# Performance work log

Hardware: AMD Instinct MI355X
Metric: run time of the kernel (lower is better)

The kernel has to match this reference:

```python
import jax, jax.numpy as jnp
import numpy as np
import math

B, S, D, H, HD = 2, 2048, 2048, 16, 128
ROPE_THETA = 10000.0


def _rope_cache(seq_len, dim, base, dtype=jnp.float32):
    inv_freq = 1.0 / (base ** (jnp.arange(0, dim, 2, dtype=jnp.float32) / dim))
    t = jnp.arange(seq_len, dtype=jnp.float32)
    freqs = jnp.einsum('i,j->ij', t, inv_freq)          # [S, dim/2]
    emb = jnp.concatenate([freqs, freqs], axis=-1)       # [S, dim]
    return jnp.cos(emb).astype(dtype), jnp.sin(emb).astype(dtype)


def _rotate_half(x):
    x1, x2 = x[..., : x.shape[-1] // 2], x[..., x.shape[-1] // 2:]
    return jnp.concatenate([-x2, x1], axis=-1)


def setup_inputs() -> dict:
    key = jax.random.key(0)
    ks = jax.random.split(key, 6)
    hidden_states = jax.random.normal(ks[0], (B, S, D), dtype=jnp.float32) * 0.02
    w_scale = 1.0 / math.sqrt(D)
    Wq = jax.random.normal(ks[1], (D, D), dtype=jnp.float32) * w_scale
    Wk = jax.random.normal(ks[2], (D, D), dtype=jnp.float32) * w_scale
    Wv = jax.random.normal(ks[3], (D, D), dtype=jnp.float32) * w_scale
    Wo = jax.random.normal(ks[4], (D, D), dtype=jnp.float32) * w_scale
    # additive causal mask [B, 1, S, S]: 0 on/below diag, large negative above
    causal = jnp.tril(jnp.ones((S, S), dtype=bool))
    attention_mask = jnp.where(causal, 0.0, -1e9).astype(jnp.float32)
    attention_mask = jnp.broadcast_to(attention_mask[None, None], (B, 1, S, S))
    position_ids = jnp.broadcast_to(jnp.arange(S, dtype=jnp.int32)[None], (B, S))
    return {
        'hidden_states': hidden_states,
        'attention_mask': attention_mask,
        'position_ids': position_ids,
        'Wq': Wq, 'Wk': Wk, 'Wv': Wv, 'Wo': Wo,
    }


def reference(hidden_states, attention_mask, position_ids, Wq, Wk, Wv, Wo):
    bsz, q_len, _ = hidden_states.shape
    # projections (torch Linear: x @ W.T), then split heads -> [B, H, S, HD]
    def proj(W):
        return jnp.einsum('bsd,ed->bse', hidden_states, W).reshape(bsz, q_len, H, HD).transpose(0, 2, 1, 3)
    q, k, v = proj(Wq), proj(Wk), proj(Wv)
    cos_c, sin_c = _rope_cache(q_len, HD, ROPE_THETA, hidden_states.dtype)
    cos = cos_c[position_ids][:, None]  # [B, 1, S, HD]
    sin = sin_c[position_ids][:, None]
    q = q * cos + _rotate_half(q) * sin
    k = k * cos + _rotate_half(k) * sin
    scores = jnp.einsum('bhqd,bhkd->bhqk', q, k) / math.sqrt(HD)
    scores = scores + attention_mask
    attn_weights = jax.nn.softmax(scores.astype(jnp.float32), axis=-1).astype(q.dtype)
    attn_out = jnp.einsum('bhqk,bhkd->bhqd', attn_weights, v)
    attn_out = attn_out.transpose(0, 2, 1, 3).reshape(bsz, q_len, D)
    out = jnp.einsum('bsd,ed->bse', attn_out, Wo)
    return out
```

## Files before the change

kernel.cpp:

```cpp
#include <hip/hip_runtime.h>

typedef __bf16 bf16;
typedef __bf16 bf16x8 __attribute__((ext_vector_type(8)));
typedef float f32x4 __attribute__((ext_vector_type(4)));

#define D_MODEL 2048
#define SEQ 2048
#define NH 16
#define HEAD_DIM 128
#define NBATCH 2
#define SM_SCALE 0.08838834764831845f
#define WSEG 4194304
#define NT_TILES 32

typedef __attribute__((address_space(1))) const void* gas_cp;
typedef __attribute__((address_space(3))) void* las_p;
__device__ __forceinline__ void ll16(const bf16* g, bf16* l) {
  __builtin_amdgcn_global_load_lds((gas_cp)g, (las_p)l, 16, 0, 0);
}

__device__ __forceinline__ bf16x8 cvt8(const float* p) {
  float4 a = *(const float4*)p;
  float4 b = *(const float4*)(p + 4);
  bf16x8 v;
  v[0] = (bf16)a.x; v[1] = (bf16)a.y; v[2] = (bf16)a.z; v[3] = (bf16)a.w;
  v[4] = (bf16)b.x; v[5] = (bf16)b.y; v[6] = (bf16)b.z; v[7] = (bf16)b.w;
  return v;
}

__global__ __launch_bounds__(256)
void cvt_hidden(const float* __restrict__ src, bf16* __restrict__ dst) {
  size_t i = ((size_t)blockIdx.x * 256 + threadIdx.x) * 8;
  *(bf16x8*)(dst + i) = cvt8(src + i);
}

__global__ __launch_bounds__(256)
void cvt_weights(const float* __restrict__ w0, const float* __restrict__ w1,
                 const float* __restrict__ w2, const float* __restrict__ w3,
                 bf16* __restrict__ dst) {
  const float* src = (blockIdx.y == 0) ? w0 : (blockIdx.y == 1) ? w1
                   : (blockIdx.y == 2) ? w2 : w3;
  size_t i = ((size_t)blockIdx.x * 256 + threadIdx.x) * 8;
  *(bf16x8*)(dst + (size_t)blockIdx.y * WSEG + i) = cvt8(src + i);
}

#define LDF256(DA, DB, SB, KX)                                               \
  _Pragma("unroll") for (int mi = 0; mi < 8; mi++)                           \
      DA[mi] = *(const bf16x8*)((SB) + ((arowQ + mi * 16) << 7) + (KX));     \
  DB[0] = *(const bf16x8*)((SB) + 32768 + (qb0 << 7) + (KX));                \
  DB[1] = *(const bf16x8*)((SB) + 32768 + (qb1 << 7) + (KX));                \
  DB[2] = *(const bf16x8*)((SB) + 32768 + (qb2 << 7) + (KX));                \
  DB[3] = *(const bf16x8*)((SB) + 32768 + (qb3 << 7) + (KX));

#define MM256(AF, BF)                                                        \
  _Pragma("unroll") for (int mi = 0; mi < 8; mi++)                           \
  _Pragma("unroll") for (int ni = 0; ni < 4; ni++)                           \
      acc[mi][ni] = __builtin_amdgcn_mfma_f32_16x16x32_bf16(                 \
          AF[mi], BF[ni], acc[mi][ni], 0, 0, 0);

#define ST2(GP, ROW0, KT, LB)                                                \
  ll16((GP) + (size_t)((ROW0) + w * 8 + l8) * D_MODEL + (KT) * 64 + kelem,   \
       (bf16*)((LB) + w * 1024));

__global__ __launch_bounds__(512, 2)
void gemm256(const bf16* __restrict__ A, const bf16* __restrict__ W,
             bf16* __restrict__ Qo, bf16* __restrict__ Ko,
             bf16* __restrict__ Vo, const int* __restrict__ pos_ids) {
  __shared__ __align__(16) char smem[131072];

  const int tid  = threadIdx.x;
  const int lane = tid & 63;
  const int w    = tid >> 6;
  const int quad = lane >> 4, l15 = lane & 15;
  const int l8   = lane >> 3, l7 = lane & 7;
  const int kelem = 8 * (l7 ^ l8);
  const int wm2 = w >> 2;
  const int wn2 = w & 3;
  const int hh  = wn2 >> 1;
  const int cb  = (wn2 & 1) * 32;

  const int bid = blockIdx.x;
  const int lin = (bid & 7) * 48 + (bid >> 3);
  const int by = lin / 24, bx = lin % 24;
  const int mBase = by << 8, nBase = bx << 8;

  const int kx0 = (quad * 16) ^ ((l15 & 7) << 4);
  const int kx1 = kx0 ^ 64;
  const int arowQ = wm2 * 128 + l15;
  const int qb0 = hh * 128 + cb + l15;
  const int qb1 = qb0 + 16, qb2 = qb0 + 64, qb3 = qb0 + 80;

  f32x4 acc[8][4];
#pragma unroll
  for (int i = 0; i < 8; i++)
#pragma unroll
    for (int j = 0; j < 4; j++) acc[i][j] = 0.0f;

  bf16x8 aP[8], bP[4];
  bf16x8 aQ[8], bQ[4];

  {
    char* s0 = smem;
    ST2(A, mBase,       0, s0 + 0);
    ST2(A, mBase + 64,  0, s0 + 8192);
    ST2(A, mBase + 128, 0, s0 + 16384);
    ST2(A, mBase + 192, 0, s0 + 24576);
    ST2(W, nBase,       0, s0 + 32768);
    ST2(W, nBase + 64,  0, s0 + 40960);
    ST2(W, nBase + 128, 0, s0 + 49152);
    ST2(W, nBase + 192, 0, s0 + 57344);
  }
  asm volatile("s_waitcnt vmcnt(0)" ::: "memory");
  __builtin_amdgcn_s_barrier();
  LDF256(aP, bP, smem, kx0);

  int buf = 0;
  for (int t = 0; t < NT_TILES; ++t) {
    char* const Sb = smem + buf * 65536;
    char* const Ob = smem + (buf ^ 1) * 65536;
    const bool pf  = (t + 1 < NT_TILES);

    LDF256(aQ, bQ, Sb, kx1);
    if (pf) {
      ST2(A, mBase,       t + 1, Ob + 0);
      ST2(A, mBase + 64,  t + 1, Ob + 8192);
      ST2(A, mBase + 128, t + 1, Ob + 16384);
      ST2(A, mBase + 192, t + 1, Ob + 24576);
      ST2(W, nBase,       t + 1, Ob + 32768);
      ST2(W, nBase + 64,  t + 1, Ob + 40960);
      ST2(W, nBase + 128, t + 1, Ob + 49152);
      ST2(W, nBase + 192, t + 1, Ob + 57344);
    }
    __builtin_amdgcn_sched_barrier(0);
    __builtin_amdgcn_s_setprio(1);
    MM256(aP, bP);
    __builtin_amdgcn_s_setprio(0);
    asm volatile("s_waitcnt lgkmcnt(0)" ::: "memory");
    asm volatile("s_waitcnt vmcnt(0)" ::: "memory");
    __builtin_amdgcn_s_barrier();

    if (pf) {
      LDF256(aP, bP, Ob, kx0);
    }
    __builtin_amdgcn_sched_barrier(0);
    __builtin_amdgcn_s_setprio(1);
    MM256(aQ, bQ);
    __builtin_amdgcn_s_setprio(0);
    asm volatile("s_waitcnt lgkmcnt(0)" ::: "memory");

    buf ^= 1;
  }

  const int matrix = nBase >> 11;
  const int nb     = nBase & 2047;
  if (matrix == 2) {
    const int h = (nb >> 7) + hh;
#pragma unroll
    for (int mi = 0; mi < 8; mi++)
#pragma unroll
      for (int ni = 0; ni < 4; ni++) {
        const int hd = cb + (ni & 1) * 16 + (ni >> 1) * 64 + l15;
#pragma unroll
        for (int r = 0; r < 4; r++) {
          int m = mBase + wm2 * 128 + mi * 16 + quad * 4 + r;
          int b = m >> 11, s2 = m & 2047;
          Vo[((size_t)((b * NH + h) * HEAD_DIM + hd)) * SEQ + s2] =
              (bf16)acc[mi][ni][r];
        }
      }
  } else {
    bf16* Out = (matrix == 0) ? Qo : Ko;
    float invf[2];
#pragma unroll
    for (int ni = 0; ni < 2; ni++)
      invf[ni] = __expf(-(float)(cb + ni * 16 + l15) *
                        (9.210340371976184f / 64.0f));
#pragma unroll
    for (int mi = 0; mi < 8; mi++)
#pragma unroll
      for (int r = 0; r < 4; r++) {
        int m = mBase + wm2 * 128 + mi * 16 + quad * 4 + r;
        float pos = (float)pos_ids[m];
        bf16* op = Out + (size_t)m * D_MODEL + nb + hh * 128 + cb + l15;
#pragma unroll
        for (int ni = 0; ni < 2; ni++) {
          float sn, cs;
          __sincosf(pos * invf[ni], &sn, &cs);
          float q0 = acc[mi][ni][r];
          float q1 = acc[mi][ni + 2][r];
          op[ni * 16]      = (bf16)(q0 * cs - q1 * sn);
          op[ni * 16 + 64] = (bf16)(q1 * cs + q0 * sn);
        }
      }
  }
}

#define LDFRAG(DA, DB, SB, KX)                                               \
  _Pragma("unroll") for (int mi = 0; mi < 4; mi++)                           \
      DA[mi] = *(const bf16x8*)((SB) + ((arow + mi * 16) << 7) + (KX));      \
  DB[0] = *(const bf16x8*)((SB) + 16384 + (rb0 << 7) + (KX));                \
  DB[1] = *(const bf16x8*)((SB) + 16384 + (rb1 << 7) + (KX));                \
  DB[2] = *(const bf16x8*)((SB) + 16384 + (rb2 << 7) + (KX));                \
  DB[3] = *(const bf16x8*)((SB) + 16384 + (rb3 << 7) + (KX));

#define MMAC(AF, BF)                                                         \
  _Pragma("unroll") for (int mi = 0; mi < 4; mi++)                           \
  _Pragma("unroll") for (int ni = 0; ni < 4; ni++)                           \
      acc[mi][ni] = __builtin_amdgcn_mfma_f32_16x16x32_bf16(                 \
          AF[mi], BF[ni], acc[mi][ni], 0, 0, 0);

#define ST1(GP, ROW0, KT, LB)                                                \
  ll16((GP) + (size_t)((ROW0) + w * 8 + l8) * D_MODEL + (KT) * 64 + kelem,   \
       (bf16*)((LB) + w * 1024));

__global__ __launch_bounds__(512, 2)
void gemm_proj(const bf16* __restrict__ A, const bf16* __restrict__ W,
               float* __restrict__ C) {
  __shared__ __align__(16) char smem[147456];

  const int tid  = threadIdx.x;
  const int lane = tid & 63;
  const int w    = tid >> 6;
  const int quad = lane >> 4, l15 = lane & 15;
  const int l8   = lane >> 3, l7 = lane & 7;
  const int kelem = 8 * (l7 ^ l8);
  const int wm = w >> 2;
  const int wn = w & 3;

  const int bid = blockIdx.x;
  const int lin = (bid & 7) * 32 + (bid >> 3);
  const int by = lin >> 3, bx = lin & 7;
  const int mBase = by << 7, nBase = bx << 8;

  const int kx0 = (quad * 16) ^ ((l15 & 7) << 4);
  const int kx1 = kx0 ^ 64;
  const int arow = wm * 64 + l15;
  const int rb0 = wn * 64 + l15;
  const int rb1 = rb0 + 16, rb2 = rb0 + 32, rb3 = rb0 + 48;

  f32x4 acc[4][4];
#pragma unroll
  for (int i = 0; i < 4; i++)
#pragma unroll
    for (int j = 0; j < 4; j++) acc[i][j] = 0.0f;

  bf16x8 aP[4], bP[4], aQ[4], bQ[4];

  {
    char* s0 = smem;
    char* s1 = smem + 49152;
    ST1(A, mBase,       0, s0 + 0);
    ST1(A, mBase + 64,  0, s0 + 8192);
    ST1(W, nBase,       0, s0 + 16384);
    ST1(W, nBase + 64,  0, s0 + 24576);
    ST1(W, nBase + 128, 0, s0 + 32768);
    ST1(W, nBase + 192, 0, s0 + 40960);
    ST1(A, mBase,       1, s1 + 0);
    ST1(A, mBase + 64,  1, s1 + 8192);
    ST1(W, nBase,       1, s1 + 16384);
    ST1(W, nBase + 64,  1, s1 + 24576);
    ST1(W, nBase + 128, 1, s1 + 32768);
    ST1(W, nBase + 192, 1, s1 + 40960);
  }
  asm volatile("s_waitcnt vmcnt(6)" ::: "memory");
  __builtin_amdgcn_s_barrier();
  LDFRAG(aP, bP, smem, kx0);

  int buf = 0;
  for (int t = 0; t < NT_TILES; ++t) {
    char* const Sb  = smem + buf * 49152;
    const int  nb1  = (buf + 1 == 3) ? 0 : buf + 1;
    const int  pb   = (buf + 2 >= 3) ? buf - 1 : buf + 2;
    char* const Nb  = smem + nb1 * 49152;
    char* const Pb  = smem + pb * 49152;
    const bool pf   = (t + 2 < NT_TILES);

    LDFRAG(aQ, bQ, Sb, kx1);
    if (pf) {
      ST1(A, mBase,      t + 2, Pb + 0);
      ST1(A, mBase + 64, t + 2, Pb + 8192);
      ST1(W, nBase,      t + 2, Pb + 16384);
    }
    __builtin_amdgcn_sched_barrier(0);
    __builtin_amdgcn_s_setprio(1);
    MMAC(aP, bP);
    __builtin_amdgcn_s_setprio(0);
    asm volatile("s_waitcnt lgkmcnt(0)" ::: "memory");
    if (pf)
      asm volatile("s_waitcnt vmcnt(3)" ::: "memory");
    else
      asm volatile("s_waitcnt vmcnt(0)" ::: "memory");
    __builtin_amdgcn_s_barrier();

    if (t + 1 < NT_TILES) {
      LDFRAG(aP, bP, Nb, kx0);
    }
    if (pf) {
      ST1(W, nBase + 64,  t + 2, Pb + 24576);
      ST1(W, nBase + 128, t + 2, Pb + 32768);
      ST1(W, nBase + 192, t + 2, Pb + 40960);
    }
    __builtin_amdgcn_sched_barrier(0);
    __builtin_amdgcn_s_setprio(1);
    MMAC(aQ, bQ);
    __builtin_amdgcn_s_setprio(0);
    asm volatile("s_waitcnt lgkmcnt(0)" ::: "memory");
    __builtin_amdgcn_s_barrier();

    buf = nb1;
  }

#pragma unroll
  for (int mi = 0; mi < 4; mi++) {
    const int m = mBase + wm * 64 + mi * 16 + quad * 4;
#pragma unroll
    for (int ni = 0; ni < 4; ni++) {
      const int n = nBase + wn * 64 + ni * 16 + l15;
      float* cp = C + (size_t)m * D_MODEL + n;
#pragma unroll
      for (int r = 0; r < 4; r++) cp[(size_t)r * D_MODEL] = acc[mi][ni][r];
    }
  }
}

__global__ __launch_bounds__(256, 1)
void attn_v3(const bf16* __restrict__ Q, const bf16* __restrict__ K,
             const bf16* __restrict__ Vt, bf16* __restrict__ O) {
  __shared__ __align__(16) bf16 Kl[2][64 * 128];
  __shared__ __align__(16) bf16 Vl[2][128 * 64];
  __shared__ __align__(16) bf16 Pl[128 * 64];

  const int tid  = threadIdx.x;
  const int lane = tid & 63;
  const int w    = tid >> 6;
  const int quad = lane >> 4, l15 = lane & 15;
  const int l8   = lane >> 3, l7 = lane & 7;
  const int jj   = blockIdx.y;
  const int bh   = blockIdx.x;
  const size_t qkBase = (size_t)(bh >> 4) * SEQ * D_MODEL + (size_t)(bh & 15) * HEAD_DIM;
  const size_t vBase  = (size_t)bh * HEAD_DIM * SEQ;
  const int kswz = (l15 & 7) << 3;
  const int prow = w * 32;

  bf16x8 ones;
#pragma unroll
  for (int i = 0; i < 8; i++) ones[i] = (bf16)1.0f;

#define STAGE_KV(T0, BUF)                                                    \
  _Pragma("unroll") for (int i_ = 0; i_ < 4; i_++) {                         \
    const int u_ = w * 4 + i_;                                               \
    const int rK = u_ * 4 + quad;                                            \
    ll16(K + qkBase + (size_t)((T0) + rK) * D_MODEL + 8 * (l15 ^ (rK & 7)),  \
         &Kl[BUF][u_ * 512]);                                                \
    const int rV = u_ * 8 + l8;                                              \
    ll16(Vt + vBase + (size_t)rV * SEQ + (T0) + 8 * (l7 ^ (rV & 7)),         \
         &Vl[BUF][u_ * 512]);                                                \
  }

#pragma unroll 1
  for (int ss = 0; ss < 2; ++ss) {
    const int s   = ss ? jj : 15 - jj;
    const int qbw = s * 128 + prow;
    const int nt  = 2 * s + 2;

    bf16x8 qa[2][4];
#pragma unroll
    for (int mi = 0; mi < 2; mi++)
#pragma unroll
      for (int kk = 0; kk < 4; kk++)
        qa[mi][kk] = *(const bf16x8*)(Q + qkBase +
            (size_t)(qbw + mi * 16 + l15) * D_MODEL + kk * 32 + quad * 8);

    f32x4 oacc[2][8], ls[2];
#pragma unroll
    for (int mi = 0; mi < 2; mi++) {
#pragma unroll
      for (int ni = 0; ni < 8; ni++) oacc[mi][ni] = 0.0f;
      ls[mi] = 0.0f;
    }

    STAGE_KV(0, 0);
    asm volatile("s_waitcnt vmcnt(0)" ::: "memory");
    __builtin_amdgcn_s_barrier();

    int cur = 0;
    for (int tt = 0; tt < nt; ++tt, cur ^= 1) {
      const int t0 = tt * 64;
      if (tt + 1 < nt) STAGE_KV(t0 + 64, cur ^ 1);

      if (t0 <= qbw + 31) {
        const bf16* Kc = &Kl[cur][0];
        const bf16* Vc = &Vl[cur][0];

        f32x4 sacc[2][4];
#pragma unroll
        for (int mi = 0; mi < 2; mi++)
#pragma unroll
          for (int ni = 0; ni < 4; ni++) sacc[mi][ni] = 0.0f;
#pragma unroll
        for (int kk = 0; kk < 4; kk++) {
#pragma unroll
          for (int ni = 0; ni < 4; ni++) {
            bf16x8 kf = *(const bf16x8*)&Kc[(ni * 16 + l15) * 128 +
                                            ((kk * 32 + quad * 8) ^ kswz)];
            sacc[0][ni] = __builtin_amdgcn_mfma_f32_16x16x32_bf16(qa[0][kk], kf, sacc[0][ni], 0, 0, 0);
            sacc[1][ni] = __builtin_amdgcn_mfma_f32_16x16x32_bf16(qa[1][kk], kf, sacc[1][ni], 0, 0, 0);
          }
        }

        if (t0 + 63 > qbw) {
#pragma unroll
          for (int mi = 0; mi < 2; mi++)
#pragma unroll
            for (int r = 0; r < 4; r++) {
              const int qrow = qbw + mi * 16 + quad * 4 + r;
              const int prr  = prow + mi * 16 + quad * 4 + r;
              const int rsw  = ((quad * 4 + r) & 7) << 3;
#pragma unroll
              for (int ni = 0; ni < 4; ni++) {
                int tcol = t0 + ni * 16 + l15;
                float pv = (tcol <= qrow)
                    ? __expf(fminf(sacc[mi][ni][r] * SM_SCALE, 30.0f)) : 0.0f;
                Pl[prr * 64 + ((ni * 16 + l15) ^ rsw)] = (bf16)pv;
              }
            }
        } else {
#pragma unroll
          for (int mi = 0; mi < 2; mi++)
#pragma unroll
            for (int r = 0; r < 4; r++) {
              const int prr = prow + mi * 16 + quad * 4 + r;
              const int rsw = ((quad * 4 + r) & 7) << 3;
#pragma unroll
              for (int ni = 0; ni < 4; ni++)
                Pl[prr * 64 + ((ni * 16 + l15) ^ rsw)] =
                    (bf16)__expf(fminf(sacc[mi][ni][r] * SM_SCALE, 30.0f));
            }
        }

#pragma unroll
        for (int kk2 = 0; kk2 < 2; kk2++) {
          const int pcol = (kk2 * 32 + quad * 8) ^ kswz;
          bf16x8 pf0 = *(const bf16x8*)&Pl[(prow + l15) * 64 + pcol];
          bf16x8 pf1 = *(const bf16x8*)&Pl[(prow + 16 + l15) * 64 + pcol];
#pragma unroll
          for (int ni = 0; ni < 8; ni++) {
            bf16x8 vf = *(const bf16x8*)&Vc[(ni * 16 + l15) * 64 + pcol];
            oacc[0][ni] = __builtin_amdgcn_mfma_f32_16x16x32_bf16(pf0, vf, oacc[0][ni], 0, 0, 0);
            oacc[1][ni] = __builtin_amdgcn_mfma_f32_16x16x32_bf16(pf1, vf, oacc[1][ni], 0, 0, 0);
          }
          ls[0] = __builtin_amdgcn_mfma_f32_16x16x32_bf16(pf0, ones, ls[0], 0, 0, 0);
          ls[1] = __builtin_amdgcn_mfma_f32_16x16x32_bf16(pf1, ones, ls[1], 0, 0, 0);
        }
      }

      asm volatile("s_waitcnt vmcnt(0)" ::: "memory");
      __builtin_amdgcn_s_barrier();
    }

#pragma unroll
    for (int mi = 0; mi < 2; mi++)
#pragma unroll
      for (int r = 0; r < 4; r++) {
        float inv = 1.0f / ls[mi][r];
        bf16* op = O + qkBase + (size_t)(qbw + mi * 16 + quad * 4 + r) * D_MODEL;
#pragma unroll
        for (int ni = 0; ni < 8; ni++)
          op[ni * 16 + l15] = (bf16)(oacc[mi][ni][r] * inv);
      }
  }
#undef STAGE_KV
}

extern "C" void kernel_launch(void* const* d_in, const int* in_sizes, int n_in,
                              void* d_out, int out_size, void* d_ws, size_t ws_size,
                              hipStream_t stream) {
  const float* hidden = (const float*)d_in[0];
  const int* pos = (const int*)d_in[2];
  const float* Wq = (const float*)d_in[3];
  const float* Wk = (const float*)d_in[4];
  const float* Wv = (const float*)d_in[5];
  const float* Wo = (const float*)d_in[6];
  float* out = (float*)d_out;

  const size_t TENS = (size_t)NBATCH * SEQ * D_MODEL;
  bf16* Qb = (bf16*)d_ws;
  bf16* Kb = Qb + TENS;
  bf16* Vt = Kb + TENS;
  bf16* AO = Vt + TENS;
  bf16* Hb = AO + TENS;
  bf16* Wb = Hb + TENS;

  cvt_hidden<<<dim3(TENS / 2048), dim3(256), 0, stream>>>(hidden, Hb);
  cvt_weights<<<dim3(WSEG / 2048, 4), dim3(256), 0, stream>>>(Wq, Wk, Wv, Wo, Wb);

  gemm256<<<dim3(384), dim3(512), 0, stream>>>(Hb, Wb, Qb, Kb, Vt, pos);

  attn_v3<<<dim3(NBATCH * NH, 8), dim3(256), 0, stream>>>(Qb, Kb, Vt, AO);

  gemm_proj<<<dim3(256), dim3(512), 0, stream>>>(
      AO, Wb + 3 * (size_t)WSEG, out);
}
```

Baseline: 377.9 us.

## Split each attention KV tile across two wave groups and reduce partial outputs

The attention kernel grows from 256 to 512 threads. The second group of four waves takes the other 32-key half of each 64-key tile, so each wave does half the QK^T and PV MFMAs per tile. The two halves' partial O accumulators and row sums are combined through shared memory at the end of each query block. The grid stays the same (256 blocks), so the aim is more waves per CU to hide latency. The cost is an extra shared-memory reduction with barriers and a larger shared-memory footprint.

```diff
diff --git a/kernel.cpp b/kernel.cpp
--- a/kernel.cpp
+++ b/kernel.cpp
@@ -323,38 +323,41 @@
   }
 }
 
-__global__ __launch_bounds__(256, 1)
-void attn_v3(const bf16* __restrict__ Q, const bf16* __restrict__ K,
+__global__ __launch_bounds__(512, 2)
+void attn_v4(const bf16* __restrict__ Q, const bf16* __restrict__ K,
              const bf16* __restrict__ Vt, bf16* __restrict__ O) {
-  __shared__ __align__(16) bf16 Kl[2][64 * 128];
-  __shared__ __align__(16) bf16 Vl[2][128 * 64];
-  __shared__ __align__(16) bf16 Pl[128 * 64];
+  __shared__ __align__(16) char smem[98304];
+  bf16* const KlB = (bf16*)smem;
+  bf16* const VlB = (bf16*)(smem + 32768);
+  bf16* const Pl  = (bf16*)(smem + 65536);
 
   const int tid  = threadIdx.x;
   const int lane = tid & 63;
   const int w    = tid >> 6;
   const int quad = lane >> 4, l15 = lane & 15;
   const int l8   = lane >> 3, l7 = lane & 7;
+  const int g    = w & 3;
+  const int h    = w >> 2;
   const int jj   = blockIdx.y;
   const int bh   = blockIdx.x;
   const size_t qkBase = (size_t)(bh >> 4) * SEQ * D_MODEL + (size_t)(bh & 15) * HEAD_DIM;
   const size_t vBase  = (size_t)bh * HEAD_DIM * SEQ;
   const int kswz = (l15 & 7) << 3;
-  const int prow = w * 32;
+  const int prow = g * 32;
 
   bf16x8 ones;
 #pragma unroll
   for (int i = 0; i < 8; i++) ones[i] = (bf16)1.0f;
 
 #define STAGE_KV(T0, BUF)                                                    \
-  _Pragma("unroll") for (int i_ = 0; i_ < 4; i_++) {                         \
-    const int u_ = w * 4 + i_;                                               \
+  _Pragma("unroll") for (int i_ = 0; i_ < 2; i_++) {                         \
+    const int u_ = w * 2 + i_;                                               \
     const int rK = u_ * 4 + quad;                                            \
     ll16(K + qkBase + (size_t)((T0) + rK) * D_MODEL + 8 * (l15 ^ (rK & 7)),  \
-         &Kl[BUF][u_ * 512]);                                                \
+         KlB + (BUF) * 8192 + u_ * 512);                                     \
     const int rV = u_ * 8 + l8;                                              \
     ll16(Vt + vBase + (size_t)rV * SEQ + (T0) + 8 * (l7 ^ (rV & 7)),         \
-         &Vl[BUF][u_ * 512]);                                                \
+         VlB + (BUF) * 8192 + u_ * 512);                                     \
   }
 
 #pragma unroll 1
@@ -389,19 +392,19 @@
       if (tt + 1 < nt) STAGE_KV(t0 + 64, cur ^ 1);
 
       if (t0 <= qbw + 31) {
-        const bf16* Kc = &Kl[cur][0];
-        const bf16* Vc = &Vl[cur][0];
-
-        f32x4 sacc[2][4];
+        const bf16* Kc = KlB + cur * 8192;
+        const bf16* Vc = VlB + cur * 8192;
+
+        f32x4 sacc[2][2];
 #pragma unroll
         for (int mi = 0; mi < 2; mi++)
 #pragma unroll
-          for (int ni = 0; ni < 4; ni++) sacc[mi][ni] = 0.0f;
+          for (int ni = 0; ni < 2; ni++) sacc[mi][ni] = 0.0f;
 #pragma unroll
         for (int kk = 0; kk < 4; kk++) {
 #pragma unroll
-          for (int ni = 0; ni < 4; ni++) {
-            bf16x8 kf = *(const bf16x8*)&Kc[(ni * 16 + l15) * 128 +
+          for (int ni = 0; ni < 2; ni++) {
+            bf16x8 kf = *(const bf16x8*)&Kc[(h * 32 + ni * 16 + l15) * 128 +
                                             ((kk * 32 + quad * 8) ^ kswz)];
             sacc[0][ni] = __builtin_amdgcn_mfma_f32_16x16x32_bf16(qa[0][kk], kf, sacc[0][ni], 0, 0, 0);
             sacc[1][ni] = __builtin_amdgcn_mfma_f32_16x16x32_bf16(qa[1][kk], kf, sacc[1][ni], 0, 0, 0);
@@ -417,11 +420,12 @@
               const int prr  = prow + mi * 16 + quad * 4 + r;
               const int rsw  = ((quad * 4 + r) & 7) << 3;
 #pragma unroll
-              for (int ni = 0; ni < 4; ni++) {
-                int tcol = t0 + ni * 16 + l15;
+              for (int ni = 0; ni < 2; ni++) {
+                const int col = h * 32 + ni * 16 + l15;
+                const int tcol = t0 + col;
                 float pv = (tcol <= qrow)
                     ? __expf(fminf(sacc[mi][ni][r] * SM_SCALE, 30.0f)) : 0.0f;
-                Pl[prr * 64 + ((ni * 16 + l15) ^ rsw)] = (bf16)pv;
+                Pl[prr * 64 + (col ^ rsw)] = (bf16)pv;
               }
             }
         } else {
@@ -432,15 +436,16 @@
               const int prr = prow + mi * 16 + quad * 4 + r;
               const int rsw = ((quad * 4 + r) & 7) << 3;
 #pragma unroll
-              for (int ni = 0; ni < 4; ni++)
-                Pl[prr * 64 + ((ni * 16 + l15) ^ rsw)] =
+              for (int ni = 0; ni < 2; ni++) {
+                const int col = h * 32 + ni * 16 + l15;
+                Pl[prr * 64 + (col ^ rsw)] =
                     (bf16)__expf(fminf(sacc[mi][ni][r] * SM_SCALE, 30.0f));
+              }
             }
         }
 
-#pragma unroll
-        for (int kk2 = 0; kk2 < 2; kk2++) {
-          const int pcol = (kk2 * 32 + quad * 8) ^ kswz;
+        {
+          const int pcol = (h * 32 + quad * 8) ^ kswz;
           bf16x8 pf0 = *(const bf16x8*)&Pl[(prow + l15) * 64 + pcol];
           bf16x8 pf1 = *(const bf16x8*)&Pl[(prow + 16 + l15) * 64 + pcol];
 #pragma unroll
@@ -458,16 +463,47 @@
       __builtin_amdgcn_s_barrier();
     }
 
-#pragma unroll
-    for (int mi = 0; mi < 2; mi++)
-#pragma unroll
-      for (int r = 0; r < 4; r++) {
-        float inv = 1.0f / ls[mi][r];
-        bf16* op = O + qkBase + (size_t)(qbw + mi * 16 + quad * 4 + r) * D_MODEL;
-#pragma unroll
-        for (int ni = 0; ni < 8; ni++)
-          op[ni * 16 + l15] = (bf16)(oacc[mi][ni][r] * inv);
+    float* const Ml = (float*)smem;
+    float* const Ls = (float*)(smem + 81920);
+    if (h == 1) {
+#pragma unroll
+      for (int mi = 0; mi < 2; mi++)
+#pragma unroll
+        for (int ni = 0; ni < 8; ni++) {
+          const int a = g * 4096 + (ni * 16 + l15) * 32 +
+                        ((mi * 16 + quad * 4) ^ ((l15 & 7) << 2));
+          *(f32x4*)&Ml[a] = oacc[mi][ni];
+        }
+      if (l15 == 0) {
+#pragma unroll
+        for (int mi = 0; mi < 2; mi++)
+#pragma unroll
+          for (int r = 0; r < 4; r++)
+            Ls[g * 32 + mi * 16 + quad * 4 + r] = ls[mi][r];
       }
+    }
+    __builtin_amdgcn_s_barrier();
+    if (h == 0) {
+#pragma unroll
+      for (int mi = 0; mi < 2; mi++) {
+        f32x4 part[8];
+#pragma unroll
+        for (int ni = 0; ni < 8; ni++) {
+          const int a = g * 4096 + (ni * 16 + l15) * 32 +
+                        ((mi * 16 + quad * 4) ^ ((l15 & 7) << 2));
+          part[ni] = *(const f32x4*)&Ml[a];
+        }
+#pragma unroll
+        for (int r = 0; r < 4; r++) {
+          const float inv = 1.0f / (ls[mi][r] + Ls[g * 32 + mi * 16 + quad * 4 + r]);
+          bf16* op = O + qkBase + (size_t)(qbw + mi * 16 + quad * 4 + r) * D_MODEL;
+#pragma unroll
+          for (int ni = 0; ni < 8; ni++)
+            op[ni * 16 + l15] = (bf16)((oacc[mi][ni][r] + part[ni][r]) * inv);
+        }
+      }
+    }
+    __builtin_amdgcn_s_barrier();
   }
 #undef STAGE_KV
 }
@@ -496,7 +532,7 @@
 
   gemm256<<<dim3(384), dim3(512), 0, stream>>>(Hb, Wb, Qb, Kb, Vt, pos);
 
-  attn_v3<<<dim3(NBATCH * NH, 8), dim3(256), 0, stream>>>(Qb, Kb, Vt, AO);
+  attn_v4<<<dim3(NBATCH * NH, 8), dim3(512), 0, stream>>>(Qb, Kb, Vt, AO);
 
   gemm_proj<<<dim3(256), dim3(512), 0, stream>>>(
       AO, Wb + 3 * (size_t)WSEG, out);
```

Measured after the change: 349.3 us. 7.6% less time.
